# Kernel tuning notes

Measured on AMD Instinct MI355X. Metric: run time of the kernel, lower is better.

Reference implementation:

```python
import jax, jax.numpy as jnp
import numpy as np


def setup_inputs() -> dict:
    key = jax.random.key(0)
    ks = jax.random.split(key, 6)
    T, n_vars, n_channels, hidden = 2048, 64, 256, 512
    # VarianceScaling(2.0,'fan_in','uniform') ~ uniform(-limit, limit), limit=sqrt(3*2/fan_in)
    limit = float(np.sqrt(3.0 * 2.0 / n_channels))
    return {
        "enriched_history": jax.random.normal(ks[0], (T, n_vars, n_channels), dtype=jnp.float32),
        "target_mask": jax.random.randint(ks[1], (n_vars,), 0, 2, dtype=jnp.int32),
        "intervention_mask": jax.random.randint(ks[2], (n_vars,), 0, 2, dtype=jnp.int32),
        "W_target": jax.random.uniform(ks[3], (n_channels, hidden), jnp.float32, -limit, limit),
        "b_target": jnp.zeros((hidden,), jnp.float32),
        "W_intervention": jax.random.uniform(ks[4], (n_channels, hidden), jnp.float32, -limit, limit),
        "b_intervention": jnp.zeros((hidden,), jnp.float32),
        "W_other": jax.random.uniform(ks[5], (n_channels, hidden), jnp.float32, -limit, limit),
        "b_other": jnp.zeros((hidden,), jnp.float32),
    }


def reference(enriched_history, target_mask, intervention_mask,
              W_target, b_target, W_intervention, b_intervention,
              W_other, b_other):
    T, n_vars, n_channels = enriched_history.shape
    tm = target_mask.astype(jnp.float32)                       # [n_vars]
    im = intervention_mask.astype(jnp.float32) * (1.0 - tm)    # exclusivity
    om = (1.0 - tm) * (1.0 - im)

    flat = enriched_history.reshape(T * n_vars, n_channels)    # [T*n_vars, C]
    proj_t = flat @ W_target + b_target                        # [T*n_vars, H]
    proj_i = flat @ W_intervention + b_intervention
    proj_o = flat @ W_other + b_other

    # Faithful to original: jnp.repeat(mask, T) -> each variable's flag repeated T times
    tm_flat = jnp.repeat(tm, T)
    im_flat = jnp.repeat(im, T)
    om_flat = jnp.repeat(om, T)

    combined = (proj_t * tm_flat[:, None]
                + proj_i * im_flat[:, None]
                + proj_o * om_flat[:, None])
    return combined.reshape(T, n_vars, -1)
```

## Files before the change

### kernel.cpp

```cpp
#include <hip/hip_runtime.h>

typedef float f32x4 __attribute__((ext_vector_type(4)));
typedef unsigned short u16x8 __attribute__((ext_vector_type(8)));
typedef __bf16 bf16x8 __attribute__((ext_vector_type(8)));
typedef __bf16 bf16x4 __attribute__((ext_vector_type(4)));

__global__ __launch_bounds__(256) void convert_w_kernel(
    const float* __restrict__ Wt_, const float* __restrict__ Wi_,
    const float* __restrict__ Wo_, unsigned short* __restrict__ out)
{
    __shared__ unsigned short tile[64][72];

    const int b    = blockIdx.x;
    const int role = b >> 5;
    const int kt   = (b & 31) >> 3;
    const int nt   = b & 7;
    const float* __restrict__ W = (role == 0) ? Wt_ : ((role == 1) ? Wi_ : Wo_);

    const int t  = threadIdx.x;
    const int r0 = t >> 4;
    const int c4 = (t & 15) << 2;

#pragma unroll
    for (int j = 0; j < 4; ++j) {
        const int kl = r0 + j * 16;
        f32x4 v = *(const f32x4*)(W + (size_t)(kt * 64 + kl) * 512 + nt * 64 + c4);
#pragma unroll
        for (int e = 0; e < 4; ++e)
            tile[c4 + e][kl] = __builtin_bit_cast(unsigned short, (__bf16)v[e]);
    }
    __syncthreads();

    const int cs = t & 7;
#pragma unroll
    for (int p = 0; p < 2; ++p) {
        const int r = (t >> 3) + p * 32;
        u16x8 v = *(const u16x8*)&tile[r][cs * 8];
        *(u16x8*)(out + (size_t)role * 512 * 256 +
                  (size_t)(nt * 64 + r) * 256 + kt * 64 + cs * 8) = v;
    }
}

__global__ __launch_bounds__(512, 4) void role_proj_kernel(
    const float* __restrict__ A,
    const int* __restrict__ tmask,
    const int* __restrict__ imask,
    const unsigned short* __restrict__ Wws,
    const float* __restrict__ bt, const float* __restrict__ bi,
    const float* __restrict__ bo,
    float* __restrict__ C)
{
    __shared__ __align__(16) unsigned char smem[64 * 1024];
    unsigned short* As = (unsigned short*)smem;

    const int tid = threadIdx.x;
    const int m0  = blockIdx.x * 64;

    const int mi   = blockIdx.x >> 5;
    const int role = tmask[mi] ? 0 : (imask[mi] ? 1 : 2);
    const unsigned short* __restrict__ W = Wws + (size_t)role * (512 * 256);
    const float* __restrict__ bias = (role == 0) ? bt : ((role == 1) ? bi : bo);

    const f32x4* abase = (const f32x4*)(A + (size_t)m0 * 256);
    f32x4 ld[8];
#pragma unroll
    for (int p = 0; p < 8; ++p)
        ld[p] = abase[tid + 512 * p];
#pragma unroll
    for (int p = 0; p < 8; ++p) {
        const int u    = tid + 512 * p;
        const int row  = u >> 6;
        const int slot = ((u & 63) >> 1) ^ (row & 7);
        bf16x4 pk = { (__bf16)ld[p][0], (__bf16)ld[p][1],
                      (__bf16)ld[p][2], (__bf16)ld[p][3] };
        *(bf16x4*)(smem + row * 512 + slot * 16 + (u & 1) * 8) = pk;
    }
    __syncthreads();

    const int lane  = tid & 63;
    const int wid   = tid >> 6;
    const int l15   = lane & 15;
    const int l4    = lane >> 4;
    const int nbase = wid * 64;
    const int r7    = l15 & 7;

    const unsigned short* wp[4];
#pragma unroll
    for (int fn = 0; fn < 4; ++fn)
        wp[fn] = W + (size_t)(nbase + fn * 16 + l15) * 256 + l4 * 8;

    f32x4 acc[4][4] = {};

#pragma unroll 1
    for (int ks = 0; ks < 8; ++ks) {
        u16x8 bfr[4];
#pragma unroll
        for (int fn = 0; fn < 4; ++fn)
            bfr[fn] = *(const u16x8*)(wp[fn] + ks * 32);
        u16x8 afr[4];
#pragma unroll
        for (int fm = 0; fm < 4; ++fm) {
            const int row  = fm * 16 + l15;
            const int slot = (ks * 4 + l4) ^ r7;
            afr[fm] = *(const u16x8*)&As[row * 256 + slot * 8];
        }
#pragma unroll
        for (int fm = 0; fm < 4; ++fm) {
#pragma unroll
            for (int fn = 0; fn < 4; ++fn) {
                acc[fm][fn] = __builtin_amdgcn_mfma_f32_16x16x32_bf16(
                    __builtin_bit_cast(bf16x8, bfr[fn]),
                    __builtin_bit_cast(bf16x8, afr[fm]),
                    acc[fm][fn], 0, 0, 0);
            }
        }
    }

    unsigned char* cs = smem + 32768 + wid * 4096;

    f32x4 bv[4];
#pragma unroll
    for (int fn = 0; fn < 4; ++fn)
        bv[fn] = *(const f32x4*)(bias + nbase + fn * 16 + l4 * 4);

#pragma unroll
    for (int fm = 0; fm < 4; ++fm) {
#pragma unroll
        for (int fn = 0; fn < 4; ++fn) {
            const int g = (fn * 4 + l4) ^ r7;
            *(f32x4*)(cs + l15 * 256 + g * 16) = acc[fm][fn] + bv[fn];
        }
#pragma unroll
        for (int q = 0; q < 4; ++q) {
            const int r = (lane >> 4) + 4 * q;
            const int g = (lane & 15) ^ (r & 7);
            f32x4 v = *(const f32x4*)(cs + r * 256 + g * 16);
            __builtin_nontemporal_store(
                v, (f32x4*)(C + (size_t)(m0 + fm * 16 + r) * 512 +
                            nbase + (lane & 15) * 4));
        }
    }
}

extern "C" void kernel_launch(void* const* d_in, const int* in_sizes, int n_in,
                              void* d_out, int out_size, void* d_ws, size_t ws_size,
                              hipStream_t stream) {
    const float* A   = (const float*)d_in[0];
    const int*   tm  = (const int*)d_in[1];
    const int*   im  = (const int*)d_in[2];
    const float* Wt_ = (const float*)d_in[3];
    const float* bt  = (const float*)d_in[4];
    const float* Wi_ = (const float*)d_in[5];
    const float* bi  = (const float*)d_in[6];
    const float* Wo_ = (const float*)d_in[7];
    const float* bo  = (const float*)d_in[8];

    unsigned short* Wws = (unsigned short*)d_ws;

    hipLaunchKernelGGL(convert_w_kernel, dim3(96), dim3(256),
                       0, stream, Wt_, Wi_, Wo_, Wws);

    hipLaunchKernelGGL(role_proj_kernel, dim3(2048), dim3(512),
                       0, stream, A, tm, im, Wws, bt, bi, bo, (float*)d_out);
}
```

Baseline: 113.2 us.

## Make projection blocks loop over four row tiles with double-buffered A prefetch

Each block now processes four consecutive 64-row tiles instead of one, so the grid shrinks to a quarter of its former size. Shared memory is split into two 32 KB buffers. The next tile's A rows are loaded from global memory while the current tile's epilogue runs, then converted to bf16 into the other buffer, which also serves as the output staging area. The aim is to overlap input loads with the MFMA work and the output stores, and to amortize per-block setup. The cost is fewer resident blocks across the CUs and an extra barrier per tile.

```diff
diff --git a/kernel.cpp b/kernel.cpp
--- a/kernel.cpp
+++ b/kernel.cpp
@@ -50,95 +50,123 @@
     const float* __restrict__ bo,
     float* __restrict__ C)
 {
-    __shared__ __align__(16) unsigned char smem[64 * 1024];
-    unsigned short* As = (unsigned short*)smem;
+    __shared__ __align__(16) unsigned char smem[2][32 * 1024];
 
-    const int tid = threadIdx.x;
-    const int m0  = blockIdx.x * 64;
+    const int tid  = threadIdx.x;
+    const int lane = tid & 63;
+    const int wid  = tid >> 6;
+    const int t0   = blockIdx.x * 4;
 
-    const int mi   = blockIdx.x >> 5;
+    const int mi   = blockIdx.x >> 3;
     const int role = tmask[mi] ? 0 : (imask[mi] ? 1 : 2);
     const unsigned short* __restrict__ W = Wws + (size_t)role * (512 * 256);
     const float* __restrict__ bias = (role == 0) ? bt : ((role == 1) ? bi : bo);
 
-    const f32x4* abase = (const f32x4*)(A + (size_t)m0 * 256);
-    f32x4 ld[8];
-#pragma unroll
-    for (int p = 0; p < 8; ++p)
-        ld[p] = abase[tid + 512 * p];
-#pragma unroll
-    for (int p = 0; p < 8; ++p) {
-        const int u    = tid + 512 * p;
-        const int row  = u >> 6;
-        const int slot = ((u & 63) >> 1) ^ (row & 7);
-        bf16x4 pk = { (__bf16)ld[p][0], (__bf16)ld[p][1],
-                      (__bf16)ld[p][2], (__bf16)ld[p][3] };
-        *(bf16x4*)(smem + row * 512 + slot * 16 + (u & 1) * 8) = pk;
-    }
-    __syncthreads();
-
-    const int lane  = tid & 63;
-    const int wid   = tid >> 6;
     const int l15   = lane & 15;
     const int l4    = lane >> 4;
     const int nbase = wid * 64;
     const int r7    = l15 & 7;
+    const int srow  = wid * 8;
 
     const unsigned short* wp[4];
 #pragma unroll
     for (int fn = 0; fn < 4; ++fn)
         wp[fn] = W + (size_t)(nbase + fn * 16 + l15) * 256 + l4 * 8;
 
-    f32x4 acc[4][4] = {};
+    {
+        const f32x4* ab = (const f32x4*)(A + (size_t)t0 * 16384) + srow * 64 + lane;
+        f32x4 ld0[8];
+#pragma unroll
+        for (int j = 0; j < 8; ++j)
+            ld0[j] = ab[j * 64];
+#pragma unroll
+        for (int j = 0; j < 8; ++j) {
+            bf16x4 pk = { (__bf16)ld0[j][0], (__bf16)ld0[j][1],
+                          (__bf16)ld0[j][2], (__bf16)ld0[j][3] };
+            const int slot = (lane >> 1) ^ j;
+            *(bf16x4*)(&smem[0][0] + (srow + j) * 512 + slot * 16 +
+                       (lane & 1) * 8) = pk;
+        }
+    }
+    asm volatile("s_waitcnt lgkmcnt(0)\n\ts_barrier" ::: "memory");
 
+    int cur = 0;
 #pragma unroll 1
-    for (int ks = 0; ks < 8; ++ks) {
-        u16x8 bfr[4];
+    for (int t = 0; t < 4; ++t) {
+        const unsigned short* As = (const unsigned short*)&smem[cur][0];
+
+        f32x4 acc[4][4] = {};
+#pragma unroll 1
+        for (int ks = 0; ks < 8; ++ks) {
+            u16x8 bfr[4];
+#pragma unroll
+            for (int fn = 0; fn < 4; ++fn)
+                bfr[fn] = *(const u16x8*)(wp[fn] + ks * 32);
+            u16x8 afr[4];
+#pragma unroll
+            for (int fm = 0; fm < 4; ++fm) {
+                const int row  = fm * 16 + l15;
+                const int slot = (ks * 4 + l4) ^ r7;
+                afr[fm] = *(const u16x8*)&As[row * 256 + slot * 8];
+            }
+#pragma unroll
+            for (int fm = 0; fm < 4; ++fm) {
+#pragma unroll
+                for (int fn = 0; fn < 4; ++fn) {
+                    acc[fm][fn] = __builtin_amdgcn_mfma_f32_16x16x32_bf16(
+                        __builtin_bit_cast(bf16x8, bfr[fn]),
+                        __builtin_bit_cast(bf16x8, afr[fm]),
+                        acc[fm][fn], 0, 0, 0);
+                }
+            }
+        }
+
+        f32x4 ld[8];
+        if (t < 3) {
+            const f32x4* ab =
+                (const f32x4*)(A + (size_t)(t0 + t + 1) * 16384) + srow * 64 + lane;
+#pragma unroll
+            for (int j = 0; j < 8; ++j)
+                ld[j] = ab[j * 64];
+        }
+
+        unsigned char* cs = &smem[cur ^ 1][0] + wid * 4096;
+        f32x4 bv[4];
 #pragma unroll
         for (int fn = 0; fn < 4; ++fn)
-            bfr[fn] = *(const u16x8*)(wp[fn] + ks * 32);
-        u16x8 afr[4];
-#pragma unroll
-        for (int fm = 0; fm < 4; ++fm) {
-            const int row  = fm * 16 + l15;
-            const int slot = (ks * 4 + l4) ^ r7;
-            afr[fm] = *(const u16x8*)&As[row * 256 + slot * 8];
-        }
+            bv[fn] = *(const f32x4*)(bias + nbase + fn * 16 + l4 * 4);
+
+        const int m0 = (t0 + t) * 64;
 #pragma unroll
         for (int fm = 0; fm < 4; ++fm) {
 #pragma unroll
             for (int fn = 0; fn < 4; ++fn) {
-                acc[fm][fn] = __builtin_amdgcn_mfma_f32_16x16x32_bf16(
-                    __builtin_bit_cast(bf16x8, bfr[fn]),
-                    __builtin_bit_cast(bf16x8, afr[fm]),
-                    acc[fm][fn], 0, 0, 0);
+                const int g = (fn * 4 + l4) ^ r7;
+                *(f32x4*)(cs + l15 * 256 + g * 16) = acc[fm][fn] + bv[fn];
+            }
+#pragma unroll
+            for (int q = 0; q < 4; ++q) {
+                const int r = (lane >> 4) + 4 * q;
+                const int g = (lane & 15) ^ (r & 7);
+                f32x4 v = *(const f32x4*)(cs + r * 256 + g * 16);
+                __builtin_nontemporal_store(
+                    v, (f32x4*)(C + (size_t)(m0 + fm * 16 + r) * 512 +
+                                nbase + (lane & 15) * 4));
             }
         }
-    }
 
-    unsigned char* cs = smem + 32768 + wid * 4096;
-
-    f32x4 bv[4];
+        if (t < 3) {
 #pragma unroll
-    for (int fn = 0; fn < 4; ++fn)
-        bv[fn] = *(const f32x4*)(bias + nbase + fn * 16 + l4 * 4);
-
-#pragma unroll
-    for (int fm = 0; fm < 4; ++fm) {
-#pragma unroll
-        for (int fn = 0; fn < 4; ++fn) {
-            const int g = (fn * 4 + l4) ^ r7;
-            *(f32x4*)(cs + l15 * 256 + g * 16) = acc[fm][fn] + bv[fn];
+            for (int j = 0; j < 8; ++j) {
+                bf16x4 pk = { (__bf16)ld[j][0], (__bf16)ld[j][1],
+                              (__bf16)ld[j][2], (__bf16)ld[j][3] };
+                const int slot = (lane >> 1) ^ j;
+                *(bf16x4*)(&smem[cur ^ 1][0] + (srow + j) * 512 + slot * 16 +
+                           (lane & 1) * 8) = pk;
+            }
         }
-#pragma unroll
-        for (int q = 0; q < 4; ++q) {
-            const int r = (lane >> 4) + 4 * q;
-            const int g = (lane & 15) ^ (r & 7);
-            f32x4 v = *(const f32x4*)(cs + r * 256 + g * 16);
-            __builtin_nontemporal_store(
-                v, (f32x4*)(C + (size_t)(m0 + fm * 16 + r) * 512 +
-                            nbase + (lane & 15) * 4));
-        }
+        asm volatile("s_waitcnt lgkmcnt(0)\n\ts_barrier" ::: "memory");
+        cur ^= 1;
     }
 }
 
@@ -160,6 +188,6 @@
     hipLaunchKernelGGL(convert_w_kernel, dim3(96), dim3(256),
                        0, stream, Wt_, Wi_, Wo_, Wws);
 
-    hipLaunchKernelGGL(role_proj_kernel, dim3(2048), dim3(512),
+    hipLaunchKernelGGL(role_proj_kernel, dim3(512), dim3(512),
                        0, stream, A, tm, im, Wws, bt, bi, bo, (float*)d_out);
 }
```

After: 147.0 us. 1.3x slower.
